# Kernel optimization log

Hardware: AMD Instinct MI355X
Metric: run time of the kernel (lower is better)

## Reference

```python
import jax, jax.numpy as jnp
import numpy as np

DIM = 1024
H = 16
D = DIM // H  # 64
EPS = 1e-6


def _rmsnorm(x, scale):
    # per-last-dim RMSNorm, computed in fp32 like the torch code
    rms = jax.lax.rsqrt(jnp.mean(x * x, axis=-1, keepdims=True) + EPS)
    return x * rms * scale


def _apply_rope(xq, xk, pe):
    # xq, xk: [B,H,L,D]; pe: [1,1,L,D/2,2,2]
    B, h, L, d = xq.shape
    xq_ = xq.reshape(B, h, L, d // 2, 1, 2)
    xk_ = xk.reshape(B, h, L, d // 2, 1, 2)
    xq_out = pe[..., 0] * xq_[..., 0] + pe[..., 1] * xq_[..., 1]  # [B,H,L,D/2,2]
    xk_out = pe[..., 0] * xk_[..., 0] + pe[..., 1] * xk_[..., 1]
    return xq_out.reshape(B, h, L, d), xk_out.reshape(B, h, L, d)


def setup_inputs() -> dict:
    key = jax.random.key(0)
    ks = jax.random.split(key, 6)
    B, L = 2, 2048
    x = jax.random.normal(ks[0], (B, L, DIM), dtype=jnp.float32)
    pe = jax.random.normal(ks[1], (1, 1, L, D // 2, 2, 2), dtype=jnp.float32)
    qkv_w = jax.random.normal(ks[2], (3 * DIM, DIM), dtype=jnp.float32) * (DIM ** -0.5)
    q_scale = jnp.ones((D,), dtype=jnp.float32)
    k_scale = jnp.ones((D,), dtype=jnp.float32)
    proj_w = jax.random.normal(ks[3], (DIM, DIM), dtype=jnp.float32) * (DIM ** -0.5)
    proj_b = jnp.zeros((DIM,), dtype=jnp.float32)
    return {"x": x, "pe": pe, "qkv_w": qkv_w, "q_scale": q_scale,
            "k_scale": k_scale, "proj_w": proj_w, "proj_b": proj_b}


def reference(x, pe, qkv_w, q_scale, k_scale, proj_w, proj_b):
    B, L, _ = x.shape
    x_c = jnp.clip(jnp.nan_to_num(x, nan=0.0, posinf=0.0, neginf=0.0), -10000.0, 10000.0)
    qkv = x_c @ qkv_w.T  # [B,L,3*DIM] (qkv_bias=False)
    qkv = jnp.nan_to_num(qkv, nan=0.0, posinf=0.0, neginf=0.0)
    # 'B L (K H D) -> K B H L D'
    qkv = qkv.reshape(B, L, 3, H, D).transpose(2, 0, 3, 1, 4)
    q, k, v = qkv[0], qkv[1], qkv[2]  # each [B,H,L,D]
    q = _rmsnorm(q, q_scale)
    k = _rmsnorm(k, k_scale)
    q, k = _apply_rope(q, k, pe)
    # scaled dot product attention (no mask)
    scores = jnp.einsum('bhqd,bhkd->bhqk', q, k) * (D ** -0.5)
    attn = jax.nn.softmax(scores, axis=-1)
    out = jnp.einsum('bhqk,bhkd->bhqd', attn, v)
    out = out.transpose(0, 2, 1, 3).reshape(B, L, H * D)  # 'B H L D -> B L (H D)'
    out = jnp.clip(out, -10000.0, 10000.0)
    return out @ proj_w.T + proj_b
```

## Files before the change

### kernel.cpp

```cpp
#include <hip/hip_runtime.h>
#include <hip/hip_bf16.h>

#define DIMC 1024
#define HEADS 16
#define HD 64
#define BATCH 2
#define SEQ 2048

typedef __bf16 bf16;
typedef __bf16 bf16x4 __attribute__((ext_vector_type(4)));
typedef __bf16 bf16x8 __attribute__((ext_vector_type(8)));
typedef float f32x4 __attribute__((ext_vector_type(4)));

typedef const __attribute__((address_space(1))) void* gas_t;
typedef __attribute__((address_space(3))) void* las_t;

__device__ inline f32x4 mfma_bf16(bf16x8 a, bf16x8 b, f32x4 c) {
    return __builtin_amdgcn_mfma_f32_16x16x32_bf16(a, b, c, 0, 0, 0);
}

__device__ inline void st8(bf16* p, bf16x8 v) {
    *(bf16x4*)p       = *(bf16x4*)&v;
    *(bf16x4*)(p + 4) = *((bf16x4*)&v + 1);
}
__device__ inline bf16x8 ld_frag(const bf16* p) {
    bf16x8 r;
    *(bf16x4*)&r       = *(const bf16x4*)p;
    *((bf16x4*)&r + 1) = *(const bf16x4*)(p + 16);
    return r;
}
__device__ inline bf16x8 ld_frag_s(const bf16* rowp, int cb, int sw) {
    bf16x8 r;
    *(bf16x4*)&r       = *(const bf16x4*)((const char*)rowp + ((cb) ^ sw));
    *((bf16x4*)&r + 1) = *(const bf16x4*)((const char*)rowp + ((cb + 32) ^ sw));
    return r;
}

__global__ __launch_bounds__(256) void k_prep_all(const float* __restrict__ x,
                                                  const float* __restrict__ qw,
                                                  const float* __restrict__ pw,
                                                  bf16* __restrict__ xb,
                                                  bf16* __restrict__ wqkv,
                                                  bf16* __restrict__ wproj) {
    int idx = blockIdx.x * 1024 + threadIdx.x;
#pragma unroll
    for (int j = 0; j < 4; ++j, idx += 256) {
        if (idx < 1048576) {
            float4 v = ((const float4*)x)[idx];
            float a[4] = {v.x, v.y, v.z, v.w};
            bf16x4 o;
#pragma unroll
            for (int q = 0; q < 4; ++q) {
                float f = a[q];
                f = __builtin_isfinite(f) ? fminf(fmaxf(f, -10000.f), 10000.f) : 0.f;
                o[q] = (bf16)f;
            }
            ((bf16x4*)xb)[idx] = o;
        } else if (idx < 1835008) {
            int i2 = idx - 1048576;
            float4 v = ((const float4*)qw)[i2];
            bf16x4 o = {(bf16)v.x, (bf16)v.y, (bf16)v.z, (bf16)v.w};
            ((bf16x4*)wqkv)[i2] = o;
        } else {
            int i2 = idx - 1835008;
            float4 v = ((const float4*)pw)[i2];
            bf16x4 o = {(bf16)v.x, (bf16)v.y, (bf16)v.z, (bf16)v.w};
            ((bf16x4*)wproj)[i2] = o;
        }
    }
}

template <bool OUT_BF16, bool BIAS, bool SANITIZE>
__global__ __launch_bounds__(256) void k_gemm_bt(const bf16* __restrict__ A,
                                                 const bf16* __restrict__ Bt,
                                                 void* __restrict__ Cv,
                                                 const float* __restrict__ bias,
                                                 int N, int K) {
    __shared__ alignas(16) bf16 As[128 * 64];
    __shared__ alignas(16) bf16 Bs[128 * 64];
    const int t = threadIdx.x;
    const int m0 = blockIdx.y * 128, n0 = blockIdx.x * 128;
    const int w = t >> 6, lane = t & 63;
    const int wm = (w >> 1) * 64, wn = (w & 1) * 64;
    const int lr = lane & 15, lg = lane >> 4;
    const int srow = lane >> 3;
    const int scol = ((lane & 7) ^ srow) * 8;
    const int sw = (lr & 7) << 4;

    f32x4 acc[4][4];
#pragma unroll
    for (int i = 0; i < 4; ++i)
#pragma unroll
        for (int j = 0; j < 4; ++j) acc[i][j] = 0.0f;

    for (int k0 = 0; k0 < K; k0 += 64) {
#pragma unroll
        for (int i = 0; i < 4; ++i) {
            int rg = w * 32 + i * 8;
            __builtin_amdgcn_global_load_lds(
                (gas_t)(A + (size_t)(m0 + rg + srow) * K + k0 + scol),
                (las_t)(As + rg * 64), 16, 0, 0);
            __builtin_amdgcn_global_load_lds(
                (gas_t)(Bt + (size_t)(n0 + rg + srow) * K + k0 + scol),
                (las_t)(Bs + rg * 64), 16, 0, 0);
        }
        __syncthreads();
#pragma unroll
        for (int kk = 0; kk < 2; ++kk) {
            const int cb = kk * 64 + lg * 8;
            bf16x8 af[4], bfr[4];
#pragma unroll
            for (int mi = 0; mi < 4; ++mi)
                af[mi] = ld_frag_s(&As[(wm + mi * 16 + lr) * 64], cb, sw);
#pragma unroll
            for (int ni = 0; ni < 4; ++ni)
                bfr[ni] = ld_frag_s(&Bs[(wn + ni * 16 + lr) * 64], cb, sw);
#pragma unroll
            for (int mi = 0; mi < 4; ++mi)
#pragma unroll
                for (int ni = 0; ni < 4; ++ni)
                    acc[mi][ni] = mfma_bf16(af[mi], bfr[ni], acc[mi][ni]);
        }
        __syncthreads();
    }
#pragma unroll
    for (int mi = 0; mi < 4; ++mi) {
#pragma unroll
        for (int ni = 0; ni < 4; ++ni) {
            int col = n0 + wn + ni * 16 + lr;
            float bval = BIAS ? bias[col] : 0.f;
#pragma unroll
            for (int r = 0; r < 4; ++r) {
                int row = m0 + wm + mi * 16 + lg * 4 + r;
                float v = acc[mi][ni][r];
                if (SANITIZE) v = __builtin_isfinite(v) ? v : 0.f;
                v += bval;
                if (OUT_BF16)
                    ((bf16*)Cv)[(size_t)row * N + col] = (bf16)v;
                else
                    ((float*)Cv)[(size_t)row * N + col] = v;
            }
        }
    }
}

__global__ __launch_bounds__(256) void k_gemm_qkv(const bf16* __restrict__ A,
                                                  const bf16* __restrict__ Bt,
                                                  const float* __restrict__ pe,
                                                  const float* __restrict__ q_scale,
                                                  const float* __restrict__ k_scale,
                                                  bf16* __restrict__ qb,
                                                  bf16* __restrict__ kb,
                                                  bf16* __restrict__ vt) {
    __shared__ alignas(16) bf16 As[128 * 64];
    __shared__ alignas(16) bf16 Bs[128 * 64];
    const int K = DIMC, t = threadIdx.x;
    const int m0 = blockIdx.y * 128, n0 = blockIdx.x * 128;
    const int w = t >> 6, lane = t & 63;
    const int wm = (w >> 1) * 64, wn = (w & 1) * 64;
    const int lr = lane & 15, lg = lane >> 4;
    const int srow = lane >> 3;
    const int scol = ((lane & 7) ^ srow) * 8;
    const int sw = (lr & 7) << 4;

    f32x4 acc[4][4];
#pragma unroll
    for (int i = 0; i < 4; ++i)
#pragma unroll
        for (int j = 0; j < 4; ++j) acc[i][j] = 0.0f;

    for (int k0 = 0; k0 < K; k0 += 64) {
#pragma unroll
        for (int i = 0; i < 4; ++i) {
            int rg = w * 32 + i * 8;
            __builtin_amdgcn_global_load_lds(
                (gas_t)(A + (size_t)(m0 + rg + srow) * K + k0 + scol),
                (las_t)(As + rg * 64), 16, 0, 0);
            __builtin_amdgcn_global_load_lds(
                (gas_t)(Bt + (size_t)(n0 + rg + srow) * K + k0 + scol),
                (las_t)(Bs + rg * 64), 16, 0, 0);
        }
        __syncthreads();
#pragma unroll
        for (int kk = 0; kk < 2; ++kk) {
            const int cb = kk * 64 + lg * 8;
            bf16x8 af[4], bfr[4];
#pragma unroll
            for (int mi = 0; mi < 4; ++mi)
                af[mi] = ld_frag_s(&As[(wm + mi * 16 + lr) * 64], cb, sw);
#pragma unroll
            for (int ni = 0; ni < 4; ++ni)
                bfr[ni] = ld_frag_s(&Bs[(wn + ni * 16 + lr) * 64], cb, sw);
#pragma unroll
            for (int mi = 0; mi < 4; ++mi)
#pragma unroll
                for (int ni = 0; ni < 4; ++ni)
                    acc[mi][ni] = mfma_bf16(af[mi], bfr[ni], acc[mi][ni]);
        }
        __syncthreads();
    }

    const int g = (n0 + wn) >> 6;
    const int sel = g >> 4;
    const int hh = g & 15;
    const int row0 = m0 + wm;
    const int bb = row0 >> 11;
    const int l0 = row0 & (SEQ - 1);
    const size_t bhh = (size_t)(bb * HEADS + hh);

#pragma unroll
    for (int mi = 0; mi < 4; ++mi)
#pragma unroll
        for (int ni = 0; ni < 4; ++ni)
#pragma unroll
            for (int r = 0; r < 4; ++r) {
                float v = acc[mi][ni][r];
                acc[mi][ni][r] = __builtin_isfinite(v) ? v : 0.f;
            }

    if (sel == 2) {
#pragma unroll
        for (int mi = 0; mi < 4; ++mi)
#pragma unroll
            for (int ni = 0; ni < 4; ++ni) {
                bf16x4 ov;
#pragma unroll
                for (int r = 0; r < 4; ++r) ov[r] = (bf16)acc[mi][ni][r];
                *(bf16x4*)(vt + (bhh * HD + ni * 16 + lr) * SEQ +
                           l0 + mi * 16 + lg * 4) = ov;
            }
    } else {
        const float* sc = sel ? k_scale : q_scale;
        bf16* dst = sel ? kb : qb;
        const float oscale = sel ? 1.0f : 0.125f * 1.44269504088896340736f;
        float scv[4];
#pragma unroll
        for (int ni = 0; ni < 4; ++ni) scv[ni] = sc[ni * 16 + lr];
#pragma unroll
        for (int mi = 0; mi < 4; ++mi) {
#pragma unroll
            for (int r = 0; r < 4; ++r) {
                float ss = 0.f;
#pragma unroll
                for (int ni = 0; ni < 4; ++ni)
                    ss += acc[mi][ni][r] * acc[mi][ni][r];
                ss += __shfl_xor(ss, 1, 64);
                ss += __shfl_xor(ss, 2, 64);
                ss += __shfl_xor(ss, 4, 64);
                ss += __shfl_xor(ss, 8, 64);
                float rms = rsqrtf(ss * (1.f / 64.f) + 1e-6f);
                int l = l0 + mi * 16 + lg * 4 + r;
                const float* peb = pe + (size_t)l * 128 + (lr & 1) * 2;
                bf16* db = dst + (bhh * SEQ + l) * HD + lr;
#pragma unroll
                for (int ni = 0; ni < 4; ++ni) {
                    float e = acc[mi][ni][r] * rms * scv[ni];
                    float p = __shfl_xor(e, 1, 64);
                    float2 pv = *(const float2*)(peb + (ni * 8 + (lr >> 1)) * 4);
                    float ee = (lr & 1) ? p : e;
                    float eo = (lr & 1) ? e : p;
                    db[ni * 16] = (bf16)((pv.x * ee + pv.y * eo) * oscale);
                }
            }
        }
    }
}

__global__ __launch_bounds__(512) void k_attn(const bf16* __restrict__ Q,
                                              const bf16* __restrict__ Kb,
                                              const bf16* __restrict__ Vt,
                                              bf16* __restrict__ O) {
    __shared__ bf16 Ks[2][64][68];
    __shared__ bf16 Vs[2][64][68];
    const int qt = blockIdx.x, bh = blockIdx.y;
    const int b = bh >> 4, h = bh & 15;
    const int t = threadIdx.x, w = t >> 6, lane = t & 63;
    const int lr = lane & 15, lg = lane >> 4;
    const size_t baseQK = (size_t)bh * SEQ * HD;
    const size_t baseVt = (size_t)bh * HD * SEQ;

    const bf16* qp = Q + baseQK + (size_t)(qt * 128 + w * 16 + lr) * HD;
    bf16x8 qf0 = ld_frag(qp + lg * 4);
    bf16x8 qf1 = ld_frag(qp + 32 + lg * 4);

    const int sr = t >> 3, scol = (t & 7) * 8;
    {
        bf16x8 kv = *(const bf16x8*)(Kb + baseQK + (size_t)sr * HD + scol);
        bf16x8 vv = *(const bf16x8*)(Vt + baseVt + (size_t)sr * SEQ + scol);
        st8(&Ks[0][sr][scol], kv);
        st8(&Vs[0][sr][scol], vv);
    }
    __syncthreads();

    bf16x8 ones;
#pragma unroll
    for (int j = 0; j < 8; ++j) ones[j] = (bf16)1.0f;

    f32x4 oacc[4];
#pragma unroll
    for (int i = 0; i < 4; ++i) oacc[i] = 0.0f;
    f32x4 lacc = 0.0f;
    float m_s = -1e30f;

    int cur = 0;
    for (int kt = 0; kt < SEQ / 64; ++kt) {
        bf16x8 kreg, vreg;
        const bool pf = (kt + 1) < SEQ / 64;
        if (pf) {
            kreg = *(const bf16x8*)(Kb + baseQK + (size_t)((kt + 1) * 64 + sr) * HD + scol);
            vreg = *(const bf16x8*)(Vt + baseVt + (size_t)sr * SEQ + (kt + 1) * 64 + scol);
        }
        __builtin_amdgcn_s_setprio(1);
        f32x4 s[4];
#pragma unroll
        for (int nk = 0; nk < 4; ++nk) {
            f32x4 a = 0.0f;
            a = mfma_bf16(ld_frag(&Ks[cur][nk * 16 + lr][lg * 4]), qf0, a);
            a = mfma_bf16(ld_frag(&Ks[cur][nk * 16 + lr][32 + lg * 4]), qf1, a);
            s[nk] = a;
        }
        __builtin_amdgcn_s_setprio(0);
        float tm = fmaxf(fmaxf(s[0][0], s[0][1]), fmaxf(s[0][2], s[0][3]));
#pragma unroll
        for (int nk = 1; nk < 4; ++nk)
            tm = fmaxf(tm, fmaxf(fmaxf(s[nk][0], s[nk][1]),
                                 fmaxf(s[nk][2], s[nk][3])));
        tm = fmaxf(tm, __shfl_xor(tm, 16, 64));
        tm = fmaxf(tm, __shfl_xor(tm, 32, 64));
        if (!__all(tm <= m_s + 8.f)) {
            float mnew = fmaxf(m_s, tm);
            float alpha = exp2f(m_s - mnew);
            m_s = mnew;
#pragma unroll
            for (int nd = 0; nd < 4; ++nd)
#pragma unroll
                for (int r2 = 0; r2 < 4; ++r2) oacc[nd][r2] *= alpha;
#pragma unroll
            for (int r2 = 0; r2 < 4; ++r2) lacc[r2] *= alpha;
        }
        bf16x8 pa0, pa1;
#pragma unroll
        for (int j = 0; j < 4; ++j) {
            pa0[j]     = (bf16)exp2f(s[0][j] - m_s);
            pa0[4 + j] = (bf16)exp2f(s[1][j] - m_s);
            pa1[j]     = (bf16)exp2f(s[2][j] - m_s);
            pa1[4 + j] = (bf16)exp2f(s[3][j] - m_s);
        }
        __builtin_amdgcn_s_setprio(1);
        lacc = mfma_bf16(ones, pa0, lacc);
        lacc = mfma_bf16(ones, pa1, lacc);
#pragma unroll
        for (int nd = 0; nd < 4; ++nd) {
            oacc[nd] = mfma_bf16(ld_frag(&Vs[cur][nd * 16 + lr][lg * 4]), pa0, oacc[nd]);
            oacc[nd] = mfma_bf16(ld_frag(&Vs[cur][nd * 16 + lr][32 + lg * 4]), pa1, oacc[nd]);
        }
        __builtin_amdgcn_s_setprio(0);
        if (pf) {
            st8(&Ks[cur ^ 1][sr][scol], kreg);
            st8(&Vs[cur ^ 1][sr][scol], vreg);
        }
        __syncthreads();
        cur ^= 1;
    }
    {
        float inv = 1.f / lacc[0];
        int q = qt * 128 + w * 16 + lr;
#pragma unroll
        for (int nd = 0; nd < 4; ++nd) {
            bf16x4 ov;
#pragma unroll
            for (int r2 = 0; r2 < 4; ++r2) {
                float v = oacc[nd][r2] * inv;
                v = fminf(fmaxf(v, -10000.f), 10000.f);
                ov[r2] = (bf16)v;
            }
            *(bf16x4*)(O + ((size_t)(b * SEQ + q)) * DIMC + h * HD + nd * 16 + lg * 4) = ov;
        }
    }
}

extern "C" void kernel_launch(void* const* d_in, const int* in_sizes, int n_in,
                              void* d_out, int out_size, void* d_ws, size_t ws_size,
                              hipStream_t stream) {
    const float* x = (const float*)d_in[0];
    const float* pe = (const float*)d_in[1];
    const float* qkv_w = (const float*)d_in[2];
    const float* q_scale = (const float*)d_in[3];
    const float* k_scale = (const float*)d_in[4];
    const float* proj_w = (const float*)d_in[5];
    const float* proj_b = (const float*)d_in[6];
    float* out = (float*)d_out;
    char* ws = (char*)d_ws;

    bf16* xb = (bf16*)(ws);
    bf16* wqkv = (bf16*)(ws + (8u << 20));
    bf16* wproj = (bf16*)(ws + (14u << 20));
    bf16* ao = (bf16*)(ws + (16u << 20));
    bf16* qb = (bf16*)(ws + (24u << 20));
    bf16* kb = (bf16*)(ws + (32u << 20));
    bf16* vt = (bf16*)(ws + (40u << 20));

    k_prep_all<<<2048, 256, 0, stream>>>(x, qkv_w, proj_w, xb, wqkv, wproj);
    k_gemm_qkv<<<dim3(24, 32), 256, 0, stream>>>(xb, wqkv, pe, q_scale, k_scale,
                                                 qb, kb, vt);
    k_attn<<<dim3(SEQ / 128, BATCH * HEADS), 512, 0, stream>>>(qb, kb, vt, ao);
    k_gemm_bt<false, true, false>
        <<<dim3(8, 32), 256, 0, stream>>>(ao, wproj, (void*)out, proj_b, 1024, 1024);
}
```

Measured before the change: 155.0 us.

## Load attention K/V tiles directly into swizzled LDS and swizzle GEMM tile order

```diff
diff --git a/kernel.cpp b/kernel.cpp
--- a/kernel.cpp
+++ b/kernel.cpp
@@ -19,10 +19,6 @@
     return __builtin_amdgcn_mfma_f32_16x16x32_bf16(a, b, c, 0, 0, 0);
 }
 
-__device__ inline void st8(bf16* p, bf16x8 v) {
-    *(bf16x4*)p       = *(bf16x4*)&v;
-    *(bf16x4*)(p + 4) = *((bf16x4*)&v + 1);
-}
 __device__ inline bf16x8 ld_frag(const bf16* p) {
     bf16x8 r;
     *(bf16x4*)&r       = *(const bf16x4*)p;
@@ -34,6 +30,14 @@
     *(bf16x4*)&r       = *(const bf16x4*)((const char*)rowp + ((cb) ^ sw));
     *((bf16x4*)&r + 1) = *(const bf16x4*)((const char*)rowp + ((cb + 32) ^ sw));
     return r;
+}
+
+__device__ inline void swz_tile(int nx, int& m0, int& n0) {
+    int flat = blockIdx.y * nx + blockIdx.x;
+    int cpx = (nx * gridDim.y) >> 3;
+    int s = (flat & 7) * cpx + (flat >> 3);
+    n0 = (s % nx) * 128;
+    m0 = (s / nx) * 128;
 }
 
 __global__ __launch_bounds__(256) void k_prep_all(const float* __restrict__ x,
@@ -79,7 +83,8 @@
     __shared__ alignas(16) bf16 As[128 * 64];
     __shared__ alignas(16) bf16 Bs[128 * 64];
     const int t = threadIdx.x;
-    const int m0 = blockIdx.y * 128, n0 = blockIdx.x * 128;
+    int m0, n0;
+    swz_tile(N >> 7, m0, n0);
     const int w = t >> 6, lane = t & 63;
     const int wm = (w >> 1) * 64, wn = (w & 1) * 64;
     const int lr = lane & 15, lg = lane >> 4;
@@ -155,7 +160,8 @@
     __shared__ alignas(16) bf16 As[128 * 64];
     __shared__ alignas(16) bf16 Bs[128 * 64];
     const int K = DIMC, t = threadIdx.x;
-    const int m0 = blockIdx.y * 128, n0 = blockIdx.x * 128;
+    int m0, n0;
+    swz_tile(24, m0, n0);
     const int w = t >> 6, lane = t & 63;
     const int wm = (w >> 1) * 64, wn = (w & 1) * 64;
     const int lr = lane & 15, lg = lane >> 4;
@@ -270,8 +276,8 @@
                                               const bf16* __restrict__ Kb,
                                               const bf16* __restrict__ Vt,
                                               bf16* __restrict__ O) {
-    __shared__ bf16 Ks[2][64][68];
-    __shared__ bf16 Vs[2][64][68];
+    __shared__ alignas(16) bf16 Ks[2][64 * 64];
+    __shared__ alignas(16) bf16 Vs[2][64 * 64];
     const int qt = blockIdx.x, bh = blockIdx.y;
     const int b = bh >> 4, h = bh & 15;
     const int t = threadIdx.x, w = t >> 6, lane = t & 63;
@@ -283,13 +289,15 @@
     bf16x8 qf0 = ld_frag(qp + lg * 4);
     bf16x8 qf1 = ld_frag(qp + 32 + lg * 4);
 
-    const int sr = t >> 3, scol = (t & 7) * 8;
-    {
-        bf16x8 kv = *(const bf16x8*)(Kb + baseQK + (size_t)sr * HD + scol);
-        bf16x8 vv = *(const bf16x8*)(Vt + baseVt + (size_t)sr * SEQ + scol);
-        st8(&Ks[0][sr][scol], kv);
-        st8(&Vs[0][sr][scol], vv);
-    }
+    const int sr = t >> 3;
+    const int sc8 = ((t & 7) ^ (sr & 7)) * 8;
+    const int wb = w * 512;
+    const bf16* kg0 = Kb + baseQK + (size_t)sr * HD + sc8;
+    const bf16* vg0 = Vt + baseVt + (size_t)sr * SEQ + sc8;
+    const int sw = (lr & 7) << 4;
+
+    __builtin_amdgcn_global_load_lds((gas_t)kg0, (las_t)(&Ks[0][wb]), 16, 0, 0);
+    __builtin_amdgcn_global_load_lds((gas_t)vg0, (las_t)(&Vs[0][wb]), 16, 0, 0);
     __syncthreads();
 
     bf16x8 ones;
@@ -304,19 +312,21 @@
 
     int cur = 0;
     for (int kt = 0; kt < SEQ / 64; ++kt) {
-        bf16x8 kreg, vreg;
-        const bool pf = (kt + 1) < SEQ / 64;
-        if (pf) {
-            kreg = *(const bf16x8*)(Kb + baseQK + (size_t)((kt + 1) * 64 + sr) * HD + scol);
-            vreg = *(const bf16x8*)(Vt + baseVt + (size_t)sr * SEQ + (kt + 1) * 64 + scol);
+        if ((kt + 1) < SEQ / 64) {
+            __builtin_amdgcn_global_load_lds(
+                (gas_t)(kg0 + (size_t)(kt + 1) * 64 * HD),
+                (las_t)(&Ks[cur ^ 1][wb]), 16, 0, 0);
+            __builtin_amdgcn_global_load_lds(
+                (gas_t)(vg0 + (kt + 1) * 64),
+                (las_t)(&Vs[cur ^ 1][wb]), 16, 0, 0);
         }
         __builtin_amdgcn_s_setprio(1);
         f32x4 s[4];
 #pragma unroll
         for (int nk = 0; nk < 4; ++nk) {
             f32x4 a = 0.0f;
-            a = mfma_bf16(ld_frag(&Ks[cur][nk * 16 + lr][lg * 4]), qf0, a);
-            a = mfma_bf16(ld_frag(&Ks[cur][nk * 16 + lr][32 + lg * 4]), qf1, a);
+            a = mfma_bf16(ld_frag_s(&Ks[cur][(nk * 16 + lr) * 64], lg * 8, sw), qf0, a);
+            a = mfma_bf16(ld_frag_s(&Ks[cur][(nk * 16 + lr) * 64], 64 + lg * 8, sw), qf1, a);
             s[nk] = a;
         }
         __builtin_amdgcn_s_setprio(0);
@@ -351,14 +361,10 @@
         lacc = mfma_bf16(ones, pa1, lacc);
 #pragma unroll
         for (int nd = 0; nd < 4; ++nd) {
-            oacc[nd] = mfma_bf16(ld_frag(&Vs[cur][nd * 16 + lr][lg * 4]), pa0, oacc[nd]);
-            oacc[nd] = mfma_bf16(ld_frag(&Vs[cur][nd * 16 + lr][32 + lg * 4]), pa1, oacc[nd]);
+            oacc[nd] = mfma_bf16(ld_frag_s(&Vs[cur][(nd * 16 + lr) * 64], lg * 8, sw), pa0, oacc[nd]);
+            oacc[nd] = mfma_bf16(ld_frag_s(&Vs[cur][(nd * 16 + lr) * 64], 64 + lg * 8, sw), pa1, oacc[nd]);
         }
         __builtin_amdgcn_s_setprio(0);
-        if (pf) {
-            st8(&Ks[cur ^ 1][sr][scol], kreg);
-            st8(&Vs[cur ^ 1][sr][scol], vreg);
-        }
         __syncthreads();
         cur ^= 1;
     }
```

Result: slower. 179.7 us (+15.9%).
